# Kernel optimization log

Hardware: AMD Instinct MI355X
Metric: run time of the kernel (lower is better)

The kernel has to match this reference:

```python
import jax, jax.numpy as jnp
import numpy as np

D_MODEL, D_FF, D_NEURON, N_HEADS = 1024, 4096, 128, 8
HEAD_DIM = D_NEURON // N_HEADS
LN_EPS = 1e-5

def gelu(x):
    return jax.nn.gelu(x, approximate=False)  # torch default is exact erf GELU

def setup_inputs() -> dict:
    key = jax.random.key(0)
    ks = jax.random.split(key, 16)
    s = 0.02
    inp = {
        "x": jax.random.normal(ks[0], (2, 2048, D_MODEL), jnp.float32),
        "neuron_patterns": jax.random.normal(ks[1], (D_FF, D_MODEL), jnp.float32) * s,
        "neuron_vecs": jax.random.normal(ks[2], (D_FF, D_NEURON), jnp.float32) * s,
        "neuron_out_dirs": jax.random.normal(ks[3], (D_FF, D_MODEL), jnp.float32) * s,
        "router_w1": jax.random.normal(ks[4], (D_MODEL, D_MODEL), jnp.float32) * s,
        "router_w2": jax.random.normal(ks[5], (D_FF, D_MODEL), jnp.float32) * s,
        "ln_g": jnp.ones((D_MODEL,), jnp.float32),
        "ln_b": jnp.zeros((D_MODEL,), jnp.float32),
        "in_proj_w": jax.random.normal(ks[6], (3 * D_NEURON, D_NEURON), jnp.float32) * s,
        "in_proj_b": jnp.zeros((3 * D_NEURON,), jnp.float32),
        "out_proj_w": jax.random.normal(ks[7], (D_NEURON, D_NEURON), jnp.float32) * s,
        "out_proj_b": jnp.zeros((D_NEURON,), jnp.float32),
        "wp1_w": jax.random.normal(ks[8], (D_NEURON // 2, D_NEURON), jnp.float32) * s,
        "wp1_b": jnp.zeros((D_NEURON // 2,), jnp.float32),
        "wp2_w": jax.random.normal(ks[9], (1, D_NEURON // 2), jnp.float32) * s,
        "wp2_b": jnp.zeros((1,), jnp.float32),
        "top_k": 32,
    }
    return inp

def _forward(x, neuron_patterns, neuron_vecs, neuron_out_dirs, router_w1, router_w2,
             ln_g, ln_b, in_proj_w, in_proj_b, out_proj_w, out_proj_b,
             wp1_w, wp1_b, wp2_w, wp2_b, top_k):
    B, S, D = x.shape
    xf = x.reshape(-1, D)                                  # [N, D]
    # Router (MLP): LayerNorm -> gelu(x @ W1^T) -> @ W2^T
    mu = jnp.mean(xf, axis=-1, keepdims=True)
    var = jnp.mean(jnp.square(xf - mu), axis=-1, keepdims=True)
    xn = (xf - mu) * jax.lax.rsqrt(var + LN_EPS) * ln_g + ln_b
    h = gelu(xn @ router_w1.T)
    scores = h @ router_w2.T                               # [N, d_ff]
    _, idx = jax.lax.top_k(scores, top_k)                  # [N, k]
    pats = neuron_patterns[idx]                            # [N, k, D]
    sems = neuron_vecs[idx]                                # [N, k, dn]
    dirs = neuron_out_dirs[idx]                            # [N, k, D]
    base = gelu(jnp.einsum('nd,nkd->nk', xf, pats))        # [N, k]
    # Small self-attention over the k gathered neuron semantics (eval: no dropout)
    qkv = sems @ in_proj_w.T + in_proj_b                   # [N, k, 3*dn]
    q, kk, v = jnp.split(qkv, 3, axis=-1)
    N, K = q.shape[0], q.shape[1]
    q = q.reshape(N, K, N_HEADS, HEAD_DIM)
    kk = kk.reshape(N, K, N_HEADS, HEAD_DIM)
    v = v.reshape(N, K, N_HEADS, HEAD_DIM)
    att = jnp.einsum('nqhd,nkhd->nhqk', q, kk) / jnp.sqrt(jnp.float32(HEAD_DIM))
    att = jax.nn.softmax(att, axis=-1)
    ao = jnp.einsum('nhqk,nkhd->nqhd', att, v).reshape(N, K, D_NEURON)
    attended = ao @ out_proj_w.T + out_proj_b              # [N, k, dn]
    # Gate: sigmoid(MLP(attended)) -> [N, k, 1]
    sw = jax.nn.sigmoid(gelu(attended @ wp1_w.T + wp1_b) @ wp2_w.T + wp2_b)
    final = base[..., None] * sw                           # [N, k, 1]
    out = jnp.einsum('nko,nkd->nd', final, dirs)           # sum over k neurons
    return out.reshape(B, S, D)

def reference(x, neuron_patterns, neuron_vecs, neuron_out_dirs, router_w1, router_w2,
              ln_g, ln_b, in_proj_w, in_proj_b, out_proj_w, out_proj_b,
              wp1_w, wp1_b, wp2_w, wp2_b, top_k):
    return _forward(x, neuron_patterns, neuron_vecs, neuron_out_dirs, router_w1, router_w2,
                    ln_g, ln_b, in_proj_w, in_proj_b, out_proj_w, out_proj_b,
                    wp1_w, wp1_b, wp2_w, wp2_b, top_k)
```

## Files before the change

kernel.cpp:

```cpp
#include <hip/hip_runtime.h>
#include <math.h>

#define N_TOK 4096
#define DM 1024
#define DFF 4096
#define DN 128
#define NH 8
#define HD 16
#define KSEL 32
#define KCAND 48
#define KMAX 64

typedef __attribute__((ext_vector_type(4))) float floatx4;
typedef __attribute__((ext_vector_type(8))) short short8;
typedef __attribute__((ext_vector_type(8))) unsigned short ushort8v;
typedef __attribute__((ext_vector_type(4))) unsigned short ushort4v;

__device__ __forceinline__ float gelu_f(float x) {
  return 0.5f * x * (1.0f + erff(x * 0.70710678118654752440f));
}
__device__ __forceinline__ float bf2f(unsigned short u) {
  union { unsigned int i; float f; } v; v.i = ((unsigned int)u) << 16; return v.f;
}
__device__ __forceinline__ unsigned short f2bf(float f) {
  unsigned int x = __float_as_uint(f);
  unsigned int r = (x + 0x7fffu + ((x >> 16) & 1u)) >> 16;
  return (unsigned short)r;
}
__device__ __forceinline__ void split3(float v, unsigned short& h, unsigned short& m,
                                       unsigned short& lo) {
  h = f2bf(v);
  float r1 = v - bf2f(h);
  m = f2bf(r1);
  float r2 = r1 - bf2f(m);
  lo = f2bf(r2);
}

__global__ __launch_bounds__(256) void ln3_kernel(const float* __restrict__ x,
    const float* __restrict__ g, const float* __restrict__ b,
    unsigned short* __restrict__ xh, unsigned short* __restrict__ xm,
    unsigned short* __restrict__ xl) {
  int n = blockIdx.x, tid = threadIdx.x;
  const float* row = x + (size_t)n * DM;
  float s = 0.f, sq = 0.f;
  for (int i = tid; i < DM; i += 256) { float v = row[i]; s += v; sq += v * v; }
  for (int off = 32; off; off >>= 1) { s += __shfl_down(s, off); sq += __shfl_down(sq, off); }
  __shared__ float ss[4], ssq[4];
  __shared__ float s_mu, s_rs;
  int wid = tid >> 6;
  if ((tid & 63) == 0) { ss[wid] = s; ssq[wid] = sq; }
  __syncthreads();
  if (tid == 0) {
    float S = ss[0] + ss[1] + ss[2] + ss[3];
    float Q = ssq[0] + ssq[1] + ssq[2] + ssq[3];
    float mu = S * (1.f / DM);
    float var = Q * (1.f / DM) - mu * mu;
    s_mu = mu; s_rs = rsqrtf(var + 1e-5f);
  }
  __syncthreads();
  float mu = s_mu, rs = s_rs;
  size_t base = (size_t)n * DM;
  for (int i = tid; i < DM; i += 256) {
    float v = (row[i] - mu) * rs * g[i] + b[i];
    unsigned short h, m, lo;
    split3(v, h, m, lo);
    xh[base + i] = h; xm[base + i] = m; xl[base + i] = lo;
  }
}

__global__ __launch_bounds__(256) void cvt_split3(const float* __restrict__ in,
    unsigned short* __restrict__ oh, unsigned short* __restrict__ om,
    unsigned short* __restrict__ ol) {
  int i = (blockIdx.x * 256 + threadIdx.x) * 4;
  float4 v = *(const float4*)(in + i);
  unsigned short h0, m0, l0, h1, m1, l1, h2, m2, l2, h3, m3, l3;
  split3(v.x, h0, m0, l0);
  split3(v.y, h1, m1, l1);
  split3(v.z, h2, m2, l2);
  split3(v.w, h3, m3, l3);
  ushort4v hh = {h0, h1, h2, h3};
  ushort4v mm = {m0, m1, m2, m3};
  ushort4v ll = {l0, l1, l2, l3};
  *(ushort4v*)(oh + i) = hh;
  *(ushort4v*)(om + i) = mm;
  *(ushort4v*)(ol + i) = ll;
}

__global__ __launch_bounds__(256) void cvt_bf16(const float* __restrict__ in,
    unsigned short* __restrict__ out) {
  int i = (blockIdx.x * 256 + threadIdx.x) * 4;
  float4 v = *(const float4*)(in + i);
  ushort4v o = {f2bf(v.x), f2bf(v.y), f2bf(v.z), f2bf(v.w)};
  *(ushort4v*)(out + i) = o;
}

__global__ __launch_bounds__(256, 1) void gemm1s(
    const unsigned short* __restrict__ Ah_, const unsigned short* __restrict__ Am_,
    const unsigned short* __restrict__ Al_, const unsigned short* __restrict__ Bh_,
    const unsigned short* __restrict__ Bm_, const unsigned short* __restrict__ Bl_,
    float* __restrict__ H, unsigned short* __restrict__ Hb) {
  __shared__ short Ahs[128 * 32], Ams[128 * 32], Als[128 * 32];
  __shared__ short Bhs[128 * 32], Bms[128 * 32], Bls[128 * 32];
  const int K = 1024;
  const int N = DM;
  int tid = threadIdx.x;
  int w = tid >> 6, l = tid & 63;
  size_t brow = (size_t)blockIdx.y * 128;
  size_t bcol = (size_t)blockIdx.x * 128;

  int r0 = w * 32 + (l >> 2);
  int g0 = (l & 3) ^ ((r0 >> 1) & 3);
  size_t oA0 = (brow + r0) * (size_t)K + g0 * 8;
  size_t oA1 = (brow + r0 + 16) * (size_t)K + g0 * 8;
  size_t oB0 = (bcol + r0) * (size_t)K + g0 * 8;
  size_t oB1 = (bcol + r0 + 16) * (size_t)K + g0 * 8;
  const short* gAh0 = (const short*)Ah_ + oA0; const short* gAh1 = (const short*)Ah_ + oA1;
  const short* gAm0 = (const short*)Am_ + oA0; const short* gAm1 = (const short*)Am_ + oA1;
  const short* gAl0 = (const short*)Al_ + oA0; const short* gAl1 = (const short*)Al_ + oA1;
  const short* gBh0 = (const short*)Bh_ + oB0; const short* gBh1 = (const short*)Bh_ + oB1;
  const short* gBm0 = (const short*)Bm_ + oB0; const short* gBm1 = (const short*)Bm_ + oB1;
  const short* gBl0 = (const short*)Bl_ + oB0; const short* gBl1 = (const short*)Bl_ + oB1;
  short* lAh = &Ahs[w * 1024]; short* lAm = &Ams[w * 1024]; short* lAl = &Als[w * 1024];
  short* lBh = &Bhs[w * 1024]; short* lBm = &Bms[w * 1024]; short* lBl = &Bls[w * 1024];

  const short8 *pah[4], *pam[4], *pal[4], *pbh[4], *pbm[4], *pbl[4];
#pragma unroll
  for (int i = 0; i < 4; i++) {
    int m = (w >> 1) * 64 + i * 16 + (l & 15);
    int slot = m * 4 + ((l >> 4) ^ ((m >> 1) & 3));
    pah[i] = (const short8*)&Ahs[slot * 8];
    pam[i] = (const short8*)&Ams[slot * 8];
    pal[i] = (const short8*)&Als[slot * 8];
    int nn = (w & 1) * 64 + i * 16 + (l & 15);
    int slotb = nn * 4 + ((l >> 4) ^ ((nn >> 1) & 3));
    pbh[i] = (const short8*)&Bhs[slotb * 8];
    pbm[i] = (const short8*)&Bms[slotb * 8];
    pbl[i] = (const short8*)&Bls[slotb * 8];
  }

  floatx4 acc[4][4];
#pragma unroll
  for (int i = 0; i < 4; i++)
#pragma unroll
    for (int j = 0; j < 4; j++) acc[i][j] = (floatx4){0.f, 0.f, 0.f, 0.f};

#define GLD(GP, LB) \
  __builtin_amdgcn_global_load_lds((const __attribute__((address_space(1))) unsigned int*)(GP), \
                                   (__attribute__((address_space(3))) unsigned int*)(LB), 16, 0, 0)

  for (int k0 = 0; k0 < K; k0 += 32) {
    __syncthreads();
    GLD(gAh0 + k0, lAh); GLD(gAh1 + k0, lAh + 512);
    GLD(gAm0 + k0, lAm); GLD(gAm1 + k0, lAm + 512);
    GLD(gAl0 + k0, lAl); GLD(gAl1 + k0, lAl + 512);
    GLD(gBh0 + k0, lBh); GLD(gBh1 + k0, lBh + 512);
    GLD(gBm0 + k0, lBm); GLD(gBm1 + k0, lBm + 512);
    GLD(gBl0 + k0, lBl); GLD(gBl1 + k0, lBl + 512);
    __syncthreads();
    short8 ah[4], am[4], al[4], bh[4], bm[4], bl[4];
#pragma unroll
    for (int i = 0; i < 4; i++) {
      ah[i] = *pah[i]; am[i] = *pam[i]; al[i] = *pal[i];
      bh[i] = *pbh[i]; bm[i] = *pbm[i]; bl[i] = *pbl[i];
    }
#pragma unroll
    for (int i = 0; i < 4; i++)
#pragma unroll
      for (int j = 0; j < 4; j++)
        acc[i][j] = __builtin_amdgcn_mfma_f32_16x16x32_bf16(ah[i], bh[j], acc[i][j], 0, 0, 0);
#pragma unroll
    for (int i = 0; i < 4; i++)
#pragma unroll
      for (int j = 0; j < 4; j++)
        acc[i][j] = __builtin_amdgcn_mfma_f32_16x16x32_bf16(am[i], bh[j], acc[i][j], 0, 0, 0);
#pragma unroll
    for (int i = 0; i < 4; i++)
#pragma unroll
      for (int j = 0; j < 4; j++)
        acc[i][j] = __builtin_amdgcn_mfma_f32_16x16x32_bf16(ah[i], bm[j], acc[i][j], 0, 0, 0);
#pragma unroll
    for (int i = 0; i < 4; i++)
#pragma unroll
      for (int j = 0; j < 4; j++)
        acc[i][j] = __builtin_amdgcn_mfma_f32_16x16x32_bf16(al[i], bh[j], acc[i][j], 0, 0, 0);
#pragma unroll
    for (int i = 0; i < 4; i++)
#pragma unroll
      for (int j = 0; j < 4; j++)
        acc[i][j] = __builtin_amdgcn_mfma_f32_16x16x32_bf16(ah[i], bl[j], acc[i][j], 0, 0, 0);
#pragma unroll
    for (int i = 0; i < 4; i++)
#pragma unroll
      for (int j = 0; j < 4; j++)
        acc[i][j] = __builtin_amdgcn_mfma_f32_16x16x32_bf16(am[i], bm[j], acc[i][j], 0, 0, 0);
  }
#undef GLD

#pragma unroll
  for (int i = 0; i < 4; i++) {
#pragma unroll
    for (int j = 0; j < 4; j++) {
#pragma unroll
      for (int r = 0; r < 4; r++) {
        size_t row = brow + (w >> 1) * 64 + i * 16 + (l >> 4) * 4 + r;
        size_t col = bcol + (w & 1) * 64 + j * 16 + (l & 15);
        float v = gelu_f(acc[i][j][r]);
        H[row * N + col] = v;
        Hb[row * N + col] = f2bf(v);
      }
    }
  }
}

__global__ __launch_bounds__(256) void gemm_bf(const unsigned short* __restrict__ Ah,
    const unsigned short* __restrict__ Bh, unsigned short* __restrict__ C) {
  __shared__ short Asd[128 * 32];
  __shared__ short Bsd[128 * 32];
  const int K = 1024;
  int tid = threadIdx.x;
  int w = tid >> 6, l = tid & 63;
  size_t brow = (size_t)blockIdx.y * 128;
  size_t bcol = (size_t)blockIdx.x * 128;
  const short* Ab = (const short*)Ah + brow * K;
  const short* Bb = (const short*)Bh + bcol * K;

  int r0 = w * 32 + (l >> 2);
  int g0 = (l & 3) ^ ((r0 >> 1) & 3);
  const short* Ag0 = Ab + (size_t)r0 * K + g0 * 8;
  const short* Ag1 = Ab + (size_t)(r0 + 16) * K + g0 * 8;
  const short* Bg0 = Bb + (size_t)r0 * K + g0 * 8;
  const short* Bg1 = Bb + (size_t)(r0 + 16) * K + g0 * 8;
  short* ALds0 = &Asd[w * 1024];
  short* ALds1 = &Asd[w * 1024 + 512];
  short* BLds0 = &Bsd[w * 1024];
  short* BLds1 = &Bsd[w * 1024 + 512];

  const short8* aptr[4];
  const short8* bptr[4];
#pragma unroll
  for (int i = 0; i < 4; i++) {
    int m = (w >> 1) * 64 + i * 16 + (l & 15);
    int slot = m * 4 + ((l >> 4) ^ ((m >> 1) & 3));
    aptr[i] = (const short8*)&Asd[slot * 8];
    int n = (w & 1) * 64 + i * 16 + (l & 15);
    int slotb = n * 4 + ((l >> 4) ^ ((n >> 1) & 3));
    bptr[i] = (const short8*)&Bsd[slotb * 8];
  }

  floatx4 acc[4][4];
#pragma unroll
  for (int i = 0; i < 4; i++)
#pragma unroll
    for (int j = 0; j < 4; j++) acc[i][j] = (floatx4){0.f, 0.f, 0.f, 0.f};

  for (int k0 = 0; k0 < K; k0 += 32) {
    __syncthreads();
    __builtin_amdgcn_global_load_lds((const __attribute__((address_space(1))) unsigned int*)(Ag0 + k0),
                                     (__attribute__((address_space(3))) unsigned int*)ALds0, 16, 0, 0);
    __builtin_amdgcn_global_load_lds((const __attribute__((address_space(1))) unsigned int*)(Ag1 + k0),
                                     (__attribute__((address_space(3))) unsigned int*)ALds1, 16, 0, 0);
    __builtin_amdgcn_global_load_lds((const __attribute__((address_space(1))) unsigned int*)(Bg0 + k0),
                                     (__attribute__((address_space(3))) unsigned int*)BLds0, 16, 0, 0);
    __builtin_amdgcn_global_load_lds((const __attribute__((address_space(1))) unsigned int*)(Bg1 + k0),
                                     (__attribute__((address_space(3))) unsigned int*)BLds1, 16, 0, 0);
    __syncthreads();
    short8 a[4], b[4];
#pragma unroll
    for (int i = 0; i < 4; i++) a[i] = *aptr[i];
#pragma unroll
    for (int j = 0; j < 4; j++) b[j] = *bptr[j];
#pragma unroll
    for (int i = 0; i < 4; i++)
#pragma unroll
      for (int j = 0; j < 4; j++)
        acc[i][j] = __builtin_amdgcn_mfma_f32_16x16x32_bf16(a[i], b[j], acc[i][j], 0, 0, 0);
  }

#pragma unroll
  for (int i = 0; i < 4; i++) {
#pragma unroll
    for (int j = 0; j < 4; j++) {
#pragma unroll
      for (int r = 0; r < 4; r++) {
        size_t row = brow + (w >> 1) * 64 + i * 16 + (l >> 4) * 4 + r;
        size_t col = bcol + (w & 1) * 64 + j * 16 + (l & 15);
        C[row * DFF + col] = f2bf(acc[i][j][r]);
      }
    }
  }
}

__global__ __launch_bounds__(256) void topk2_kernel(const unsigned short* __restrict__ scores,
    int* __restrict__ cand, int* __restrict__ cnt) {
  int wv = threadIdx.x >> 6, l = threadIdx.x & 63;
  int n = blockIdx.x * 4 + wv;
  const ushort8v* row = (const ushort8v*)(scores + (size_t)n * DFF);
  unsigned short key[64];
#pragma unroll
  for (int i = 0; i < 8; i++) {
    ushort8v v = row[l * 8 + i];
#pragma unroll
    for (int e = 0; e < 8; e++) {
      unsigned short u = v[e];
      key[i * 8 + e] = (u & 0x8000u) ? (unsigned short)(~u)
                                     : (unsigned short)(u | 0x8000u);
    }
  }
  unsigned int prefix = 0;
#pragma unroll
  for (int bit = 15; bit >= 0; bit--) {
    unsigned int probe = prefix | (1u << bit);
    int c = 0;
#pragma unroll
    for (int i = 0; i < 64; i++) c += (key[i] >= probe) ? 1 : 0;
#pragma unroll
    for (int s = 1; s < 64; s <<= 1) c += __shfl_xor(c, s);
    if (c >= KCAND) prefix = probe;
  }
  unsigned short thr = (unsigned short)prefix;
  unsigned long long ltmask = (1ull << l) - 1ull;
  int base = 0;
  int* outp = cand + (size_t)n * KMAX;
#pragma unroll
  for (int i = 0; i < 64; i++) {
    bool p = key[i] >= thr;
    unsigned long long m = __ballot(p);
    if (p) {
      int pos = base + __popcll(m & ltmask);
      if (pos < KMAX) outp[pos] = l * 64 + i;
    }
    base += __popcll(m);
  }
  if (l == 0) cnt[n] = base < KMAX ? base : KMAX;
}

__global__ __launch_bounds__(256) void rescore_kernel(const float* __restrict__ h,
    const float* __restrict__ w2f, const int* __restrict__ cand,
    const int* __restrict__ cnt, int* __restrict__ idx32) {
  __shared__ float sh[DM];
  __shared__ float sc[KMAX];
  __shared__ int sidx[KMAX];
  __shared__ int s_cnt;
  int n = blockIdx.x, tid = threadIdx.x;
  *(float4*)&sh[tid * 4] = *(const float4*)(h + (size_t)n * DM + tid * 4);
  if (tid == 0) s_cnt = cnt[n];
  if (tid < KMAX) { sidx[tid] = cand[(size_t)n * KMAX + tid]; sc[tid] = -INFINITY; }
  __syncthreads();
  int cntv = s_cnt;
  int w = tid >> 6, lane = tid & 63;
  for (int c = w; c < cntv; c += 4) {
    const float4* row = (const float4*)(w2f + (size_t)sidx[c] * DM);
    const float4* hp = (const float4*)sh;
    float s = 0.f;
#pragma unroll
    for (int t = 0; t < 4; t++) {
      float4 wv = row[t * 64 + lane];
      float4 hv = hp[t * 64 + lane];
      s = fmaf(wv.x, hv.x, s); s = fmaf(wv.y, hv.y, s);
      s = fmaf(wv.z, hv.z, s); s = fmaf(wv.w, hv.w, s);
    }
    for (int off = 32; off; off >>= 1) s += __shfl_xor(s, off);
    if (lane == 0) sc[c] = s;
  }
  __syncthreads();
  if (tid < cntv) {
    float st = sc[tid]; int it = sidx[tid];
    int rank = 0;
    for (int j = 0; j < KMAX; j++) {
      float sj = sc[j];
      rank += (sj > st) || (sj == st && sidx[j] < it);
    }
    if (rank < KSEL) idx32[(size_t)n * KSEL + rank] = it;
  }
}

__global__ __launch_bounds__(384) void qkvtab_kernel(const float* __restrict__ nv,
    const float* __restrict__ ipw, const float* __restrict__ ipb,
    unsigned short* __restrict__ tab) {
  __shared__ float s_nv[8 * 128];
  int f0 = blockIdx.x * 8;
  int tid = threadIdx.x;
  for (int i = tid; i < 8 * 128; i += 384) s_nv[i] = nv[(size_t)f0 * 128 + i];
  __syncthreads();
  int row = tid;
  float bias = ipb[row];
  float acc[8];
#pragma unroll
  for (int ff = 0; ff < 8; ff++) acc[ff] = bias;
  const float* wr = ipw + (size_t)row * 128;
  for (int c = 0; c < 128; c++) {
    float w = wr[c];
#pragma unroll
    for (int ff = 0; ff < 8; ff++) acc[ff] = fmaf(s_nv[ff * 128 + c], w, acc[ff]);
  }
#pragma unroll
  for (int ff = 0; ff < 8; ff++) tab[(size_t)(f0 + ff) * 384 + row] = f2bf(acc[ff]);
}

#define KVS 132
#define AOS 132
__global__ __launch_bounds__(256) void tail6_kernel(
    const float* __restrict__ xf, const unsigned short* __restrict__ pats_b,
    const unsigned short* __restrict__ dirs_b, const unsigned short* __restrict__ qtab_b,
    const int* __restrict__ idxs,
    const unsigned short* __restrict__ opwb, const float* __restrict__ opb,
    const unsigned short* __restrict__ w1b, const float* __restrict__ b1,
    const float* __restrict__ w2, const float* __restrict__ b2,
    float* __restrict__ out) {
  __shared__ float s_k[32 * KVS];
  __shared__ float s_v[32 * KVS];
  __shared__ float s_base[32];
  __shared__ float s_coef[32];
  __shared__ int s_idx[32];
  unsigned short* s_ao = (unsigned short*)s_k;
  unsigned short* s_at = (unsigned short*)s_v;

  int n = blockIdx.x, tid = threadIdx.x;
  int w = tid >> 6, l = tid & 63;

  if (tid < 32) s_idx[tid] = idxs[(size_t)n * 32 + tid];
  __syncthreads();

#pragma unroll
  for (int p = 0; p < 4; p++) {
    int i = p * 256 + tid;
    int j = i >> 5, c = i & 31;
    int half = c >> 4, cc = c & 15;
    ushort8v v = *(const ushort8v*)(qtab_b + (size_t)s_idx[j] * 384 + 128 + half * 128 + cc * 8);
    float4 f0 = {bf2f(v[0]), bf2f(v[1]), bf2f(v[2]), bf2f(v[3])};
    float4 f1 = {bf2f(v[4]), bf2f(v[5]), bf2f(v[6]), bf2f(v[7])};
    float* dst = (half ? s_v : s_k) + j * KVS + cc * 8;
    *(float4*)dst = f0;
    *(float4*)(dst + 4) = f1;
  }

  {
    int j = tid >> 3, g = tid & 7;
    const ushort8v* pr = (const ushort8v*)(pats_b + (size_t)s_idx[j] * DM);
    const float4* xr = (const float4*)(xf + (size_t)n * DM);
    float s = 0.f;
#pragma unroll 4
    for (int it = 0; it < 16; it++) {
      int ch = it * 8 + g;
      ushort8v pv = pr[ch];
      float4 xv0 = xr[ch * 2];
      float4 xv1 = xr[ch * 2 + 1];
      s = fmaf(bf2f(pv[0]), xv0.x, s); s = fmaf(bf2f(pv[1]), xv0.y, s);
      s = fmaf(bf2f(pv[2]), xv0.z, s); s = fmaf(bf2f(pv[3]), xv0.w, s);
      s = fmaf(bf2f(pv[4]), xv1.x, s); s = fmaf(bf2f(pv[5]), xv1.y, s);
      s = fmaf(bf2f(pv[6]), xv1.z, s); s = fmaf(bf2f(pv[7]), xv1.w, s);
    }
    s += __shfl_xor(s, 1);
    s += __shfl_xor(s, 2);
    s += __shfl_xor(s, 4);
    if (g == 0) s_base[j] = gelu_f(s);
  }
  __syncthreads();

  float att[32];
  int qj = l & 31;
  int h0 = w * 2 + (l >> 5);
  {
    const ushort8v* qr = (const ushort8v*)(qtab_b + (size_t)s_idx[qj] * 384 + h0 * 16);
    ushort8v q0 = qr[0], q1 = qr[1];
    float q[16];
#pragma unroll
    for (int e = 0; e < 8; e++) { q[e] = bf2f(q0[e]); q[8 + e] = bf2f(q1[e]); }
#pragma unroll 8
    for (int kj = 0; kj < 32; kj++) {
      const float4* kr = (const float4*)&s_k[kj * KVS + h0 * 16];
      float4 k0 = kr[0], k1 = kr[1], k2 = kr[2], k3 = kr[3];
      float s = 0.f;
      s = fmaf(q[0], k0.x, s);  s = fmaf(q[1], k0.y, s);
      s = fmaf(q[2], k0.z, s);  s = fmaf(q[3], k0.w, s);
      s = fmaf(q[4], k1.x, s);  s = fmaf(q[5], k1.y, s);
      s = fmaf(q[6], k1.z, s);  s = fmaf(q[7], k1.w, s);
      s = fmaf(q[8], k2.x, s);  s = fmaf(q[9], k2.y, s);
      s = fmaf(q[10], k2.z, s); s = fmaf(q[11], k2.w, s);
      s = fmaf(q[12], k3.x, s); s = fmaf(q[13], k3.y, s);
      s = fmaf(q[14], k3.z, s); s = fmaf(q[15], k3.w, s);
      att[kj] = s * 0.25f;
    }
    float m = att[0];
#pragma unroll
    for (int k = 1; k < 32; k++) m = fmaxf(m, att[k]);
    float sum = 0.f;
#pragma unroll
    for (int k = 0; k < 32; k++) { att[k] = expf(att[k] - m); sum += att[k]; }
    float inv = 1.f / sum;
#pragma unroll
    for (int k = 0; k < 32; k++) att[k] *= inv;
  }
  __syncthreads();

  {
    float o[16];
#pragma unroll
    for (int e = 0; e < 16; e++) o[e] = 0.f;
#pragma unroll 8
    for (int kj = 0; kj < 32; kj++) {
      const float4* vr = (const float4*)&s_v[kj * KVS + h0 * 16];
      float4 v0 = vr[0], v1 = vr[1], v2 = vr[2], v3 = vr[3];
      float a = att[kj];
      o[0] = fmaf(a, v0.x, o[0]);   o[1] = fmaf(a, v0.y, o[1]);
      o[2] = fmaf(a, v0.z, o[2]);   o[3] = fmaf(a, v0.w, o[3]);
      o[4] = fmaf(a, v1.x, o[4]);   o[5] = fmaf(a, v1.y, o[5]);
      o[6] = fmaf(a, v1.z, o[6]);   o[7] = fmaf(a, v1.w, o[7]);
      o[8] = fmaf(a, v2.x, o[8]);   o[9] = fmaf(a, v2.y, o[9]);
      o[10] = fmaf(a, v2.z, o[10]); o[11] = fmaf(a, v2.w, o[11]);
      o[12] = fmaf(a, v3.x, o[12]); o[13] = fmaf(a, v3.y, o[13]);
      o[14] = fmaf(a, v3.z, o[14]); o[15] = fmaf(a, v3.w, o[15]);
    }
    ushort8v o0, o1;
#pragma unroll
    for (int e = 0; e < 8; e++) { o0[e] = f2bf(o[e]); o1[e] = f2bf(o[8 + e]); }
    ushort8v* ao = (ushort8v*)&s_ao[qj * AOS + h0 * 16];
    ao[0] = o0; ao[1] = o1;
  }
  __syncthreads();

  {
    floatx4 acc[4];
#pragma unroll
    for (int nt = 0; nt < 4; nt++) acc[nt] = (floatx4){0.f, 0.f, 0.f, 0.f};
    int rbase = (w & 1) * 16;
    int cblk = (w >> 1) * 4;
#pragma unroll
    for (int kst = 0; kst < 4; kst++) {
      short8 a = *(const short8*)&s_ao[(rbase + (l & 15)) * AOS + kst * 32 + (l >> 4) * 8];
#pragma unroll
      for (int nt = 0; nt < 4; nt++) {
        short8 b = *(const short8*)&opwb[(size_t)((cblk + nt) * 16 + (l & 15)) * 128 + kst * 32 + (l >> 4) * 8];
        acc[nt] = __builtin_amdgcn_mfma_f32_16x16x32_bf16(a, b, acc[nt], 0, 0, 0);
      }
    }
#pragma unroll
    for (int nt = 0; nt < 4; nt++) {
      int col = (cblk + nt) * 16 + (l & 15);
      float bias = opb[col];
#pragma unroll
      for (int r = 0; r < 4; r++) {
        int row = rbase + (l >> 4) * 4 + r;
        s_at[row * AOS + col] = f2bf(acc[nt][r] + bias);
      }
    }
  }
  __syncthreads();

  if (w < 2) {
    floatx4 acc[4];
#pragma unroll
    for (int nt = 0; nt < 4; nt++) acc[nt] = (floatx4){0.f, 0.f, 0.f, 0.f};
#pragma unroll
    for (int kst = 0; kst < 4; kst++) {
      short8 a = *(const short8*)&s_at[(w * 16 + (l & 15)) * AOS + kst * 32 + (l >> 4) * 8];
#pragma unroll
      for (int nt = 0; nt < 4; nt++) {
        short8 b = *(const short8*)&w1b[(size_t)(nt * 16 + (l & 15)) * 128 + kst * 32 + (l >> 4) * 8];
        acc[nt] = __builtin_amdgcn_mfma_f32_16x16x32_bf16(a, b, acc[nt], 0, 0, 0);
      }
    }
    float p[4] = {0.f, 0.f, 0.f, 0.f};
#pragma unroll
    for (int nt = 0; nt < 4; nt++) {
      int col = nt * 16 + (l & 15);
      float bb = b1[col], ww = w2[col];
#pragma unroll
      for (int r = 0; r < 4; r++)
        p[r] = fmaf(gelu_f(acc[nt][r] + bb), ww, p[r]);
    }
#pragma unroll
    for (int r = 0; r < 4; r++) {
      p[r] += __shfl_xor(p[r], 1);
      p[r] += __shfl_xor(p[r], 2);
      p[r] += __shfl_xor(p[r], 4);
      p[r] += __shfl_xor(p[r], 8);
    }
    if ((l & 15) == 0) {
      float b2v = b2[0];
#pragma unroll
      for (int r = 0; r < 4; r++) {
        int row = w * 16 + (l >> 4) * 4 + r;
        float sw = 1.f / (1.f + expf(-(p[r] + b2v)));
        s_coef[row] = s_base[row] * sw;
      }
    }
  }
  __syncthreads();

  {
    int d0 = tid * 4;
    float4 a = {0.f, 0.f, 0.f, 0.f};
#pragma unroll 8
    for (int j = 0; j < 32; j++) {
      float c = s_coef[j];
      ushort4v dv = *(const ushort4v*)&dirs_b[(size_t)s_idx[j] * DM + d0];
      a.x = fmaf(c, bf2f(dv.x), a.x);
      a.y = fmaf(c, bf2f(dv.y), a.y);
      a.z = fmaf(c, bf2f(dv.z), a.z);
      a.w = fmaf(c, bf2f(dv.w), a.w);
    }
    *(float4*)&out[(size_t)n * 1024 + d0] = a;
  }
}

extern "C" void kernel_launch(void* const* d_in, const int* in_sizes, int n_in,
                              void* d_out, int out_size, void* d_ws, size_t ws_size,
                              hipStream_t stream) {
  const float* x    = (const float*)d_in[0];
  const float* pats = (const float*)d_in[1];
  const float* nv   = (const float*)d_in[2];
  const float* dirs = (const float*)d_in[3];
  const float* rw1  = (const float*)d_in[4];
  const float* rw2  = (const float*)d_in[5];
  const float* lng  = (const float*)d_in[6];
  const float* lnb  = (const float*)d_in[7];
  const float* ipw  = (const float*)d_in[8];
  const float* ipb  = (const float*)d_in[9];
  const float* opw  = (const float*)d_in[10];
  const float* opb  = (const float*)d_in[11];
  const float* w1   = (const float*)d_in[12];
  const float* b1   = (const float*)d_in[13];
  const float* w2   = (const float*)d_in[14];
  const float* b2   = (const float*)d_in[15];
  float* out = (float*)d_out;

  const size_t MB = 1u << 20;
  char* ws = (char*)d_ws;
  unsigned short* xnh  = (unsigned short*)(ws + 0);
  unsigned short* xnm  = (unsigned short*)(ws + 8 * MB);
  float* h             = (float*)(ws + 16 * MB);
  unsigned short* sb   = (unsigned short*)(ws + 32 * MB);
  unsigned short* w1h  = (unsigned short*)(ws + 32 * MB);
  unsigned short* w1m  = (unsigned short*)(ws + 34 * MB);
  unsigned short* w1l  = (unsigned short*)(ws + 36 * MB);
  unsigned short* xnl  = (unsigned short*)(ws + 38 * MB);
  unsigned short* qtab = (unsigned short*)(ws + 64 * MB);
  unsigned short* hb   = (unsigned short*)(ws + 67 * MB);
  unsigned short* w2b  = (unsigned short*)(ws + 75 * MB);
  unsigned short* patsb= (unsigned short*)(ws + 83 * MB);
  unsigned short* dirsb= (unsigned short*)(ws + 91 * MB);
  unsigned short* opwb = (unsigned short*)(ws + 99 * MB);
  unsigned short* w1b  = (unsigned short*)(ws + 99 * MB + 64 * 1024);
  int* idx32           = (int*)(ws + 100 * MB);
  int* cand            = (int*)(ws + 101 * MB);
  int* cnt             = (int*)(ws + 102 * MB);

  ln3_kernel<<<N_TOK, 256, 0, stream>>>(x, lng, lnb, xnh, xnm, xnl);
  cvt_split3<<<(DM * DM) / 1024, 256, 0, stream>>>(rw1, w1h, w1m, w1l);
  gemm1s<<<dim3(DM / 128, N_TOK / 128), 256, 0, stream>>>(xnh, xnm, xnl, w1h, w1m, w1l, h, hb);
  cvt_bf16<<<(DFF * DM) / 1024, 256, 0, stream>>>(rw2, w2b);
  cvt_bf16<<<(DFF * DM) / 1024, 256, 0, stream>>>(pats, patsb);
  cvt_bf16<<<(DFF * DM) / 1024, 256, 0, stream>>>(dirs, dirsb);
  cvt_bf16<<<(DN * DN) / 1024, 256, 0, stream>>>(opw, opwb);
  cvt_bf16<<<(DN * DN / 2) / 1024, 256, 0, stream>>>(w1, w1b);
  gemm_bf<<<dim3(DFF / 128, N_TOK / 128), 256, 0, stream>>>(hb, w2b, sb);
  topk2_kernel<<<N_TOK / 4, 256, 0, stream>>>(sb, cand, cnt);
  rescore_kernel<<<N_TOK, 256, 0, stream>>>(h, rw2, cand, cnt, idx32);
  qkvtab_kernel<<<DFF / 8, 384, 0, stream>>>(nv, ipw, ipb, qtab);
  tail6_kernel<<<N_TOK, 256, 0, stream>>>(x, patsb, dirsb, qtab, idx32,
                                          opwb, opb, w1b, b1, w2, b2, out);
}
```

Measured before the change: 519.4 us.

## Split router GEMM1 along K into two partials and add a GELU combine kernel

The first router GEMM (three-way split bf16 emulation of the fp32 matmul) is split along K into two halves using a third grid dimension. The launch-bounds limit of one block per CU is removed, so more blocks can be resident to hide memory latency. Each half writes fp32 partial sums to workspace. A new elementwise kernel adds the two partials, applies GELU and writes both the fp32 and bf16 activations. Workspace buffers are moved around so the partials fit, at the cost of extra global traffic for the partials and one more launch.

```diff
diff --git a/kernel.cpp b/kernel.cpp
--- a/kernel.cpp
+++ b/kernel.cpp
@@ -94,11 +94,26 @@
   *(ushort4v*)(out + i) = o;
 }
 
-__global__ __launch_bounds__(256, 1) void gemm1s(
+__global__ __launch_bounds__(256) void combine_kernel(const float* __restrict__ p0,
+    const float* __restrict__ p1, float* __restrict__ H, unsigned short* __restrict__ Hb) {
+  int i = (blockIdx.x * 256 + threadIdx.x) * 4;
+  float4 a = *(const float4*)(p0 + i);
+  float4 b = *(const float4*)(p1 + i);
+  float4 v;
+  v.x = gelu_f(a.x + b.x);
+  v.y = gelu_f(a.y + b.y);
+  v.z = gelu_f(a.z + b.z);
+  v.w = gelu_f(a.w + b.w);
+  *(float4*)(H + i) = v;
+  ushort4v o = {f2bf(v.x), f2bf(v.y), f2bf(v.z), f2bf(v.w)};
+  *(ushort4v*)(Hb + i) = o;
+}
+
+__global__ __launch_bounds__(256) void gemm1s(
     const unsigned short* __restrict__ Ah_, const unsigned short* __restrict__ Am_,
     const unsigned short* __restrict__ Al_, const unsigned short* __restrict__ Bh_,
     const unsigned short* __restrict__ Bm_, const unsigned short* __restrict__ Bl_,
-    float* __restrict__ H, unsigned short* __restrict__ Hb) {
+    float* __restrict__ Hpart) {
   __shared__ short Ahs[128 * 32], Ams[128 * 32], Als[128 * 32];
   __shared__ short Bhs[128 * 32], Bms[128 * 32], Bls[128 * 32];
   const int K = 1024;
@@ -107,6 +122,8 @@
   int w = tid >> 6, l = tid & 63;
   size_t brow = (size_t)blockIdx.y * 128;
   size_t bcol = (size_t)blockIdx.x * 128;
+  int koff = blockIdx.z * 512;
+  float* Hp = Hpart + (size_t)blockIdx.z * N_TOK * DM;
 
   int r0 = w * 32 + (l >> 2);
   int g0 = (l & 3) ^ ((r0 >> 1) & 3);
@@ -148,7 +165,7 @@
   __builtin_amdgcn_global_load_lds((const __attribute__((address_space(1))) unsigned int*)(GP), \
                                    (__attribute__((address_space(3))) unsigned int*)(LB), 16, 0, 0)
 
-  for (int k0 = 0; k0 < K; k0 += 32) {
+  for (int k0 = koff; k0 < koff + 512; k0 += 32) {
     __syncthreads();
     GLD(gAh0 + k0, lAh); GLD(gAh1 + k0, lAh + 512);
     GLD(gAm0 + k0, lAm); GLD(gAm1 + k0, lAm + 512);
@@ -204,9 +221,7 @@
       for (int r = 0; r < 4; r++) {
         size_t row = brow + (w >> 1) * 64 + i * 16 + (l >> 4) * 4 + r;
         size_t col = bcol + (w & 1) * 64 + j * 16 + (l & 15);
-        float v = gelu_f(acc[i][j][r]);
-        H[row * N + col] = v;
-        Hb[row * N + col] = f2bf(v);
+        Hp[row * N + col] = acc[i][j][r];
       }
     }
   }
@@ -630,14 +645,16 @@
   unsigned short* xnh  = (unsigned short*)(ws + 0);
   unsigned short* xnm  = (unsigned short*)(ws + 8 * MB);
   float* h             = (float*)(ws + 16 * MB);
+  float* p0            = (float*)(ws + 32 * MB);
+  float* p1            = (float*)(ws + 48 * MB);
   unsigned short* sb   = (unsigned short*)(ws + 32 * MB);
-  unsigned short* w1h  = (unsigned short*)(ws + 32 * MB);
-  unsigned short* w1m  = (unsigned short*)(ws + 34 * MB);
-  unsigned short* w1l  = (unsigned short*)(ws + 36 * MB);
-  unsigned short* xnl  = (unsigned short*)(ws + 38 * MB);
   unsigned short* qtab = (unsigned short*)(ws + 64 * MB);
   unsigned short* hb   = (unsigned short*)(ws + 67 * MB);
+  unsigned short* w1h  = (unsigned short*)(ws + 67 * MB);
+  unsigned short* w1m  = (unsigned short*)(ws + 69 * MB);
+  unsigned short* w1l  = (unsigned short*)(ws + 71 * MB);
   unsigned short* w2b  = (unsigned short*)(ws + 75 * MB);
+  unsigned short* xnl  = (unsigned short*)(ws + 75 * MB);
   unsigned short* patsb= (unsigned short*)(ws + 83 * MB);
   unsigned short* dirsb= (unsigned short*)(ws + 91 * MB);
   unsigned short* opwb = (unsigned short*)(ws + 99 * MB);
@@ -648,7 +665,8 @@
 
   ln3_kernel<<<N_TOK, 256, 0, stream>>>(x, lng, lnb, xnh, xnm, xnl);
   cvt_split3<<<(DM * DM) / 1024, 256, 0, stream>>>(rw1, w1h, w1m, w1l);
-  gemm1s<<<dim3(DM / 128, N_TOK / 128), 256, 0, stream>>>(xnh, xnm, xnl, w1h, w1m, w1l, h, hb);
+  gemm1s<<<dim3(DM / 128, N_TOK / 128, 2), 256, 0, stream>>>(xnh, xnm, xnl, w1h, w1m, w1l, p0);
+  combine_kernel<<<(N_TOK * DM) / 1024, 256, 0, stream>>>(p0, p1, h, hb);
   cvt_bf16<<<(DFF * DM) / 1024, 256, 0, stream>>>(rw2, w2b);
   cvt_bf16<<<(DFF * DM) / 1024, 256, 0, stream>>>(pats, patsb);
   cvt_bf16<<<(DFF * DM) / 1024, 256, 0, stream>>>(dirs, dirsb);
```

After: 499.8 us. -3.8%, faster.
